# Kernel tuning notes

Hardware: AMD Instinct MI355X
Metric: run time of the kernel (lower is better)

Reference implementation:

```python
import jax, jax.numpy as jnp
import numpy as np

T, D_IN, D_OUT, E = 8192, 1024, 1024, 8
LN_EPS = 1e-5


def setup_inputs() -> dict:
    key = jax.random.key(0)
    k1, k2, k3 = jax.random.split(key, 3)
    x = jax.random.normal(k1, (T, D_IN), dtype=jnp.float32)
    # tokens are pre-sorted by expert; equal load => capacity = T // E per expert
    expert_frequency = jnp.full((E,), T // E, dtype=jnp.int64)
    # per-expert Linear(input_dim, output_dim) params
    W = jax.random.normal(k2, (E, D_IN, D_OUT), dtype=jnp.float32) / np.sqrt(D_IN)
    b = jax.random.normal(k3, (E, D_OUT), dtype=jnp.float32) * 0.02
    # per-expert LayerNorm(output_dim) affine params
    ln_gamma = jnp.ones((E, D_OUT), dtype=jnp.float32)
    ln_beta = jnp.zeros((E, D_OUT), dtype=jnp.float32)
    return {
        "expert_ordered_input": x,
        "expert_frequency": expert_frequency,
        "W": W,
        "b": b,
        "ln_gamma": ln_gamma,
        "ln_beta": ln_beta,
    }


def reference(expert_ordered_input, expert_frequency, W, b, ln_gamma, ln_beta):
    # Grouped-GEMM form of: split tokens by expert_frequency, apply per-expert
    # LayerBlock (Linear -> relu -> LayerNorm), then concat along token dim.
    # Frequencies are equal (capacity = T // E), so the ragged split is a reshape.
    x = expert_ordered_input
    n_tok, d_in = x.shape
    n_exp = W.shape[0]
    cap = n_tok // n_exp  # static capacity per expert
    xe = x.reshape(n_exp, cap, d_in)                       # [E, cap, d_in]
    h = jnp.einsum("ecd,edf->ecf", xe, W) + b[:, None, :]  # [E, cap, d_out]
    h = jax.nn.relu(h)
    mu = jnp.mean(h, axis=-1, keepdims=True)
    var = jnp.var(h, axis=-1, keepdims=True)
    hn = (h - mu) * jax.lax.rsqrt(var + LN_EPS)
    out = hn * ln_gamma[:, None, :] + ln_beta[:, None, :]
    return out.reshape(n_tok, -1)                          # concat over experts
```

## Files before the change

kernel.cpp:

```cpp
#include <hip/hip_runtime.h>
#include <hip/hip_bf16.h>
#include <stdint.h>

#define T_TOK 8192
#define DIN   1024
#define DOUT  1024
#define NEXP  8
#define CAP   1024
#define LN_EPS 1e-5f

#define BM 128
#define BN 128
#define BK 32
#define LDSS 48

typedef __attribute__((ext_vector_type(8))) short short8;
typedef __attribute__((ext_vector_type(4))) float f32x4;

__device__ __forceinline__ unsigned short f2bf(float f) {
    union { float f; unsigned int u; } v; v.f = f;
    unsigned int u = v.u;
    unsigned int r = u + 0x7FFFu + ((u >> 16) & 1u);
    return (unsigned short)(r >> 16);
}

__device__ __forceinline__ void gld16(void* l, const void* g) {
    __builtin_amdgcn_global_load_lds(
        (const __attribute__((address_space(1))) unsigned int*)(uintptr_t)g,
        (__attribute__((address_space(3))) unsigned int*)(uintptr_t)l,
        16, 0, 0);
}

__global__ __launch_bounds__(256) void xb_kernel(const float* __restrict__ X,
                                                 unsigned short* __restrict__ Xb) {
    int i = blockIdx.x * 256 + threadIdx.x;
    float4 v = ((const float4*)X)[i];
    ushort4 o;
    o.x = f2bf(v.x); o.y = f2bf(v.y); o.z = f2bf(v.z); o.w = f2bf(v.w);
    ((ushort4*)Xb)[i] = o;
}

__global__ __launch_bounds__(256) void wt_kernel(const float* __restrict__ W,
                                                 unsigned short* __restrict__ Wt) {
    __shared__ float tile[32][33];
    int e  = blockIdx.z;
    int k0 = blockIdx.y * 32;
    int n0 = blockIdx.x * 32;
    const float* Wp = W + (size_t)e * DIN * DOUT;
    unsigned short* Wtp = Wt + (size_t)e * DIN * DOUT;
    int tid = threadIdx.x;
    {
        int k  = tid >> 3;
        int c4 = tid & 7;
        float4 v = *(const float4*)(Wp + (size_t)(k0 + k) * DOUT + n0 + c4 * 4);
        tile[k][c4 * 4 + 0] = v.x; tile[k][c4 * 4 + 1] = v.y;
        tile[k][c4 * 4 + 2] = v.z; tile[k][c4 * 4 + 3] = v.w;
    }
    __syncthreads();
    {
        int n  = tid >> 3;
        int kc = tid & 7;
        ushort4 o;
        o.x = f2bf(tile[kc * 4 + 0][n]);
        o.y = f2bf(tile[kc * 4 + 1][n]);
        o.z = f2bf(tile[kc * 4 + 2][n]);
        o.w = f2bf(tile[kc * 4 + 3][n]);
        *(ushort4*)(Wtp + (size_t)(n0 + n) * DIN + k0 + kc * 4) = o;
    }
}

__global__ __launch_bounds__(256) void gemm2_kernel(
    const unsigned short* __restrict__ Xb,
    const unsigned short* __restrict__ Wt,
    const float* __restrict__ Bias,
    float* __restrict__ H)
{
    __shared__ unsigned short As[BM * BK];
    __shared__ unsigned short Bs[BN * BK];

    int blk = blockIdx.x;
    int e   = blk & 7;
    int m0  = (blk >> 6) * BM;
    int n0  = ((blk >> 3) & 7) * BN;

    int tid  = threadIdx.x;
    int wave = tid >> 6;
    int lane = tid & 63;
    int wm   = (wave >> 1) * 64;
    int wn   = (wave & 1) * 64;
    int lrow = lane & 15;
    int quad = lane >> 4;

    const unsigned short* Ag = Xb + (size_t)(e * CAP + m0) * DIN;
    const unsigned short* Bg = Wt + (size_t)e * DOUT * DIN + (size_t)n0 * DIN;

    int l0 = tid;
    int l1 = tid + 256;
    int ar0 = l0 >> 2, ac0 = (l0 & 3) * 8;
    int ar1 = l1 >> 2, ac1 = (l1 & 3) * 8;

    f32x4 acc[4][4];
#pragma unroll
    for (int i = 0; i < 4; i++)
#pragma unroll
        for (int j = 0; j < 4; j++)
            acc[i][j] = (f32x4)(0.0f);

    for (int k0 = 0; k0 < DIN; k0 += BK) {
        gld16(&As[l0 * 8], Ag + (size_t)ar0 * DIN + k0 + ac0);
        gld16(&As[l1 * 8], Ag + (size_t)ar1 * DIN + k0 + ac1);
        gld16(&Bs[l0 * 8], Bg + (size_t)ar0 * DIN + k0 + ac0);
        gld16(&Bs[l1 * 8], Bg + (size_t)ar1 * DIN + k0 + ac1);
        __syncthreads();

        short8 af[4], bf[4];
#pragma unroll
        for (int i = 0; i < 4; i++)
            af[i] = *(const short8*)&As[(wm + i * 16 + lrow) * BK + quad * 8];
#pragma unroll
        for (int j = 0; j < 4; j++)
            bf[j] = *(const short8*)&Bs[(wn + j * 16 + lrow) * BK + quad * 8];
#pragma unroll
        for (int i = 0; i < 4; i++)
#pragma unroll
            for (int j = 0; j < 4; j++)
                acc[i][j] = __builtin_amdgcn_mfma_f32_16x16x32_bf16(af[i], bf[j], acc[i][j], 0, 0, 0);
        __syncthreads();
    }

    float bias[4];
#pragma unroll
    for (int j = 0; j < 4; j++)
        bias[j] = Bias[e * DOUT + n0 + wn + j * 16 + lrow];

    int tok0 = e * CAP + m0 + wm;
#pragma unroll
    for (int i = 0; i < 4; i++) {
#pragma unroll
        for (int j = 0; j < 4; j++) {
            int col = n0 + wn + j * 16 + lrow;
#pragma unroll
            for (int r = 0; r < 4; r++) {
                int row = tok0 + i * 16 + quad * 4 + r;
                float v = acc[i][j][r] + bias[j];
                H[(size_t)row * DOUT + col] = fmaxf(v, 0.0f);
            }
        }
    }
}

__global__ __launch_bounds__(256, 2) void gemm_fb_kernel(
    const float* __restrict__ X,
    const unsigned short* __restrict__ Wt,
    const float* __restrict__ Bias,
    float* __restrict__ H)
{
    __shared__ unsigned short As[BM * LDSS];
    __shared__ unsigned short Bs[BN * LDSS];
    int blk = blockIdx.x;
    int e   = blk >> 6;
    int tt  = blk & 63;
    int m0  = (tt >> 3) * BM;
    int n0  = (tt & 7) * BN;
    int tid  = threadIdx.x;
    int wave = tid >> 6;
    int lane = tid & 63;
    int wm   = (wave >> 1) * 64;
    int wn   = (wave & 1) * 64;
    int lrow = lane & 15;
    int quad = lane >> 4;
    const float* Xe = X + (size_t)(e * CAP + m0) * DIN;
    const unsigned short* We = Wt + (size_t)e * DOUT * DIN + (size_t)n0 * DIN;
    f32x4 acc[4][4];
#pragma unroll
    for (int i = 0; i < 4; i++)
#pragma unroll
        for (int j = 0; j < 4; j++)
            acc[i][j] = (f32x4)(0.0f);
    for (int k0 = 0; k0 < DIN; k0 += BK) {
#pragma unroll
        for (int i = 0; i < 4; i++) {
            int idx = tid + i * 256;
            int row = idx >> 3;
            int c4  = idx & 7;
            const float4 xv = *(const float4*)(Xe + (size_t)row * DIN + k0 + c4 * 4);
            ushort4 bv;
            bv.x = f2bf(xv.x); bv.y = f2bf(xv.y); bv.z = f2bf(xv.z); bv.w = f2bf(xv.w);
            *(ushort4*)&As[row * LDSS + c4 * 4] = bv;
        }
#pragma unroll
        for (int i = 0; i < 2; i++) {
            int idx = tid + i * 256;
            int row = idx >> 2;
            int c   = idx & 3;
            uint4 wv = *(const uint4*)(We + (size_t)row * DIN + k0 + c * 8);
            *(uint4*)&Bs[row * LDSS + c * 8] = wv;
        }
        __syncthreads();
        short8 af[4], bf[4];
#pragma unroll
        for (int i = 0; i < 4; i++)
            af[i] = *(const short8*)&As[(wm + i * 16 + lrow) * LDSS + quad * 8];
#pragma unroll
        for (int j = 0; j < 4; j++)
            bf[j] = *(const short8*)&Bs[(wn + j * 16 + lrow) * LDSS + quad * 8];
#pragma unroll
        for (int i = 0; i < 4; i++)
#pragma unroll
            for (int j = 0; j < 4; j++)
                acc[i][j] = __builtin_amdgcn_mfma_f32_16x16x32_bf16(af[i], bf[j], acc[i][j], 0, 0, 0);
        __syncthreads();
    }
    float bias[4];
#pragma unroll
    for (int j = 0; j < 4; j++)
        bias[j] = Bias[e * DOUT + n0 + wn + j * 16 + lrow];
    int tok0 = e * CAP + m0 + wm;
#pragma unroll
    for (int i = 0; i < 4; i++)
#pragma unroll
        for (int j = 0; j < 4; j++) {
            int col = n0 + wn + j * 16 + lrow;
#pragma unroll
            for (int r = 0; r < 4; r++) {
                int row = tok0 + i * 16 + quad * 4 + r;
                float v = acc[i][j][r] + bias[j];
                H[(size_t)row * DOUT + col] = fmaxf(v, 0.0f);
            }
        }
}

__global__ __launch_bounds__(256) void ln_kernel(float* __restrict__ H,
                                                 const float* __restrict__ G,
                                                 const float* __restrict__ Bt) {
    int row = blockIdx.x;
    int e   = row >> 10;
    int tid  = threadIdx.x;
    int wave = tid >> 6;
    int lane = tid & 63;
    float* hp = H + (size_t)row * DOUT;

    float4 x = *(const float4*)(hp + tid * 4);
    float s  = x.x + x.y + x.z + x.w;
    float ss = fmaf(x.x, x.x, fmaf(x.y, x.y, fmaf(x.z, x.z, x.w * x.w)));
#pragma unroll
    for (int m = 32; m >= 1; m >>= 1) {
        s  += __shfl_xor(s, m);
        ss += __shfl_xor(ss, m);
    }
    __shared__ float red[8];
    if (lane == 0) { red[wave] = s; red[4 + wave] = ss; }
    __syncthreads();
    float ts  = red[0] + red[1] + red[2] + red[3];
    float tss = red[4] + red[5] + red[6] + red[7];
    float mean = ts * (1.0f / DOUT);
    float var  = fmaxf(tss * (1.0f / DOUT) - mean * mean, 0.0f);
    float rs = rsqrtf(var + LN_EPS);
    float4 g = *(const float4*)(G  + (size_t)e * DOUT + tid * 4);
    float4 b = *(const float4*)(Bt + (size_t)e * DOUT + tid * 4);
    float4 y;
    y.x = (x.x - mean) * rs * g.x + b.x;
    y.y = (x.y - mean) * rs * g.y + b.y;
    y.z = (x.z - mean) * rs * g.z + b.z;
    y.w = (x.w - mean) * rs * g.w + b.w;
    *(float4*)(hp + tid * 4) = y;
}

extern "C" void kernel_launch(void* const* d_in, const int* in_sizes, int n_in,
                              void* d_out, int out_size, void* d_ws, size_t ws_size,
                              hipStream_t stream) {
    const float* x  = (const float*)d_in[0];
    const float* W  = (const float*)d_in[2];
    const float* b  = (const float*)d_in[3];
    const float* g  = (const float*)d_in[4];
    const float* be = (const float*)d_in[5];
    float* out = (float*)d_out;

    unsigned short* Wt = (unsigned short*)d_ws;
    const size_t WT_BYTES = (size_t)NEXP * DIN * DOUT * 2;
    const size_t XB_BYTES = (size_t)T_TOK * DIN * 2;

    dim3 tb(256);
    wt_kernel<<<dim3(32, 32, 8), tb, 0, stream>>>(W, Wt);

    if (ws_size >= WT_BYTES + XB_BYTES) {
        unsigned short* Xb = (unsigned short*)((char*)d_ws + WT_BYTES);
        xb_kernel<<<dim3(8192), tb, 0, stream>>>(x, Xb);
        gemm2_kernel<<<dim3(512), tb, 0, stream>>>(Xb, Wt, b, out);
    } else {
        gemm_fb_kernel<<<dim3(512), tb, 0, stream>>>(x, Wt, b, out);
    }
    ln_kernel<<<dim3(8192), tb, 0, stream>>>(out, g, be);
}
```

Baseline: 153.0 us.

## Fuse LayerNorm into GEMM epilogue via atomic row stats and strip barrier

Merges the bf16 conversion of X and W plus zeroing of the stats buffers into one prep launch. The GEMM epilogue now applies bias and ReLU, accumulates per-row sum and sum-of-squares with atomics, and waits on a per-strip counter until all 8 N-tiles of that row strip have contributed. It then writes the normalized output directly, which removes the separate LayerNorm pass and the write and re-read of H. The inter-block spin-wait assumes all 8 blocks of a strip are co-resident (512 blocks at 2 per CU), so the code risks deadlock and adds atomic contention.

```diff
diff --git a/kernel.cpp b/kernel.cpp
--- a/kernel.cpp
+++ b/kernel.cpp
@@ -31,57 +31,70 @@
         16, 0, 0);
 }
 
-__global__ __launch_bounds__(256) void xb_kernel(const float* __restrict__ X,
-                                                 unsigned short* __restrict__ Xb) {
-    int i = blockIdx.x * 256 + threadIdx.x;
-    float4 v = ((const float4*)X)[i];
-    ushort4 o;
-    o.x = f2bf(v.x); o.y = f2bf(v.y); o.z = f2bf(v.z); o.w = f2bf(v.w);
-    ((ushort4*)Xb)[i] = o;
-}
-
-__global__ __launch_bounds__(256) void wt_kernel(const float* __restrict__ W,
-                                                 unsigned short* __restrict__ Wt) {
+__global__ __launch_bounds__(256) void prep_kernel(
+    const float* __restrict__ X, const float* __restrict__ W,
+    unsigned short* __restrict__ Xb, unsigned short* __restrict__ Wt,
+    float4* __restrict__ stats4, int* __restrict__ ctr) {
     __shared__ float tile[32][33];
-    int e  = blockIdx.z;
-    int k0 = blockIdx.y * 32;
-    int n0 = blockIdx.x * 32;
-    const float* Wp = W + (size_t)e * DIN * DOUT;
-    unsigned short* Wtp = Wt + (size_t)e * DIN * DOUT;
+    int blk = blockIdx.x;
     int tid = threadIdx.x;
-    {
-        int k  = tid >> 3;
-        int c4 = tid & 7;
-        float4 v = *(const float4*)(Wp + (size_t)(k0 + k) * DOUT + n0 + c4 * 4);
-        tile[k][c4 * 4 + 0] = v.x; tile[k][c4 * 4 + 1] = v.y;
-        tile[k][c4 * 4 + 2] = v.z; tile[k][c4 * 4 + 3] = v.w;
-    }
-    __syncthreads();
-    {
-        int n  = tid >> 3;
-        int kc = tid & 7;
+    if (blk < 8192) {
+        int i = blk * 256 + tid;
+        float4 v = ((const float4*)X)[i];
         ushort4 o;
-        o.x = f2bf(tile[kc * 4 + 0][n]);
-        o.y = f2bf(tile[kc * 4 + 1][n]);
-        o.z = f2bf(tile[kc * 4 + 2][n]);
-        o.w = f2bf(tile[kc * 4 + 3][n]);
-        *(ushort4*)(Wtp + (size_t)(n0 + n) * DIN + k0 + kc * 4) = o;
-    }
-}
-
-__global__ __launch_bounds__(256) void gemm2_kernel(
+        o.x = f2bf(v.x); o.y = f2bf(v.y); o.z = f2bf(v.z); o.w = f2bf(v.w);
+        ((ushort4*)Xb)[i] = o;
+    } else if (blk < 16384) {
+        int t  = blk - 8192;
+        int e  = t >> 10;
+        int k0 = ((t >> 5) & 31) * 32;
+        int n0 = (t & 31) * 32;
+        const float* Wp = W + (size_t)e * DIN * DOUT;
+        unsigned short* Wtp = Wt + (size_t)e * DIN * DOUT;
+        {
+            int k  = tid >> 3;
+            int c4 = tid & 7;
+            float4 v = *(const float4*)(Wp + (size_t)(k0 + k) * DOUT + n0 + c4 * 4);
+            tile[k][c4 * 4 + 0] = v.x; tile[k][c4 * 4 + 1] = v.y;
+            tile[k][c4 * 4 + 2] = v.z; tile[k][c4 * 4 + 3] = v.w;
+        }
+        __syncthreads();
+        {
+            int n  = tid >> 3;
+            int kc = tid & 7;
+            ushort4 o;
+            o.x = f2bf(tile[kc * 4 + 0][n]);
+            o.y = f2bf(tile[kc * 4 + 1][n]);
+            o.z = f2bf(tile[kc * 4 + 2][n]);
+            o.w = f2bf(tile[kc * 4 + 3][n]);
+            *(ushort4*)(Wtp + (size_t)(n0 + n) * DIN + k0 + kc * 4) = o;
+        }
+    } else {
+        int z = blk - 16384;
+        stats4[z * 256 + tid] = make_float4(0.f, 0.f, 0.f, 0.f);
+        if (z == 0 && tid < 64) ctr[tid] = 0;
+    }
+}
+
+__global__ __launch_bounds__(256, 2) void gemm3_kernel(
     const unsigned short* __restrict__ Xb,
     const unsigned short* __restrict__ Wt,
     const float* __restrict__ Bias,
-    float* __restrict__ H)
+    const float* __restrict__ G,
+    const float* __restrict__ Bt,
+    float* __restrict__ stats,
+    int* __restrict__ ctr,
+    float* __restrict__ Out)
 {
     __shared__ unsigned short As[BM * BK];
     __shared__ unsigned short Bs[BN * BK];
 
     int blk = blockIdx.x;
     int e   = blk & 7;
-    int m0  = (blk >> 6) * BM;
+    int mi  = blk >> 6;
+    int m0  = mi * BM;
     int n0  = ((blk >> 3) & 7) * BN;
+    int strip = e * 8 + mi;
 
     int tid  = threadIdx.x;
     int wave = tid >> 6;
@@ -128,32 +141,74 @@
         __syncthreads();
     }
 
-    float bias[4];
-#pragma unroll
-    for (int j = 0; j < 4; j++)
-        bias[j] = Bias[e * DOUT + n0 + wn + j * 16 + lrow];
+    float bias[4], gg[4], bb[4];
+#pragma unroll
+    for (int j = 0; j < 4; j++) {
+        int col = e * DOUT + n0 + wn + j * 16 + lrow;
+        bias[j] = Bias[col];
+        gg[j]   = G[col];
+        bb[j]   = Bt[col];
+    }
 
     int tok0 = e * CAP + m0 + wm;
+
 #pragma unroll
     for (int i = 0; i < 4; i++) {
 #pragma unroll
-        for (int j = 0; j < 4; j++) {
-            int col = n0 + wn + j * 16 + lrow;
-#pragma unroll
-            for (int r = 0; r < 4; r++) {
-                int row = tok0 + i * 16 + quad * 4 + r;
-                float v = acc[i][j][r] + bias[j];
-                H[(size_t)row * DOUT + col] = fmaxf(v, 0.0f);
+        for (int r = 0; r < 4; r++) {
+            float s = 0.f, ss = 0.f;
+#pragma unroll
+            for (int j = 0; j < 4; j++) {
+                float v = fmaxf(acc[i][j][r] + bias[j], 0.f);
+                acc[i][j][r] = v;
+                s += v;
+                ss = fmaf(v, v, ss);
+            }
+#pragma unroll
+            for (int m = 1; m <= 8; m <<= 1) {
+                s  += __shfl_xor(s, m);
+                ss += __shfl_xor(ss, m);
+            }
+            if (lrow == 0) {
+                int grow = tok0 + i * 16 + quad * 4 + r;
+                unsafeAtomicAdd(&stats[2 * grow],     s);
+                unsafeAtomicAdd(&stats[2 * grow + 1], ss);
+            }
+        }
+    }
+
+    __syncthreads();
+    if (tid == 0) {
+        __threadfence();
+        atomicAdd(&ctr[strip], 1);
+        while (atomicAdd(&ctr[strip], 0) < 8)
+            __builtin_amdgcn_s_sleep(8);
+    }
+    __syncthreads();
+    __threadfence();
+
+#pragma unroll
+    for (int i = 0; i < 4; i++) {
+#pragma unroll
+        for (int r = 0; r < 4; r++) {
+            int grow = tok0 + i * 16 + quad * 4 + r;
+            float su = stats[2 * grow];
+            float sq = stats[2 * grow + 1];
+            float mu  = su * (1.0f / DOUT);
+            float var = fmaxf(sq * (1.0f / DOUT) - mu * mu, 0.f);
+            float rs  = rsqrtf(var + LN_EPS);
+#pragma unroll
+            for (int j = 0; j < 4; j++) {
+                int gcol = n0 + wn + j * 16 + lrow;
+                Out[(size_t)grow * DOUT + gcol] = (acc[i][j][r] - mu) * rs * gg[j] + bb[j];
             }
         }
     }
 }
 
 __global__ __launch_bounds__(256, 2) void gemm_fb_kernel(
-    const float* __restrict__ X,
-    const unsigned short* __restrict__ Wt,
-    const float* __restrict__ Bias,
-    float* __restrict__ H)
+    const float* __restrict__ X, const unsigned short* __restrict__ Wt,
+    const float* __restrict__ Bias, float* __restrict__ H)
 {
     __shared__ unsigned short As[BM * LDSS];
     __shared__ unsigned short Bs[BN * LDSS];
@@ -239,7 +294,6 @@
     int wave = tid >> 6;
     int lane = tid & 63;
     float* hp = H + (size_t)row * DOUT;
-
     float4 x = *(const float4*)(hp + tid * 4);
     float s  = x.x + x.y + x.z + x.w;
     float ss = fmaf(x.x, x.x, fmaf(x.y, x.y, fmaf(x.z, x.z, x.w * x.w)));
@@ -266,6 +320,36 @@
     *(float4*)(hp + tid * 4) = y;
 }
 
+__global__ __launch_bounds__(256) void wt_only_kernel(const float* __restrict__ W,
+                                                      unsigned short* __restrict__ Wt) {
+    __shared__ float tile[32][33];
+    int t  = blockIdx.x;
+    int e  = t >> 10;
+    int k0 = ((t >> 5) & 31) * 32;
+    int n0 = (t & 31) * 32;
+    int tid = threadIdx.x;
+    const float* Wp = W + (size_t)e * DIN * DOUT;
+    unsigned short* Wtp = Wt + (size_t)e * DIN * DOUT;
+    {
+        int k  = tid >> 3;
+        int c4 = tid & 7;
+        float4 v = *(const float4*)(Wp + (size_t)(k0 + k) * DOUT + n0 + c4 * 4);
+        tile[k][c4 * 4 + 0] = v.x; tile[k][c4 * 4 + 1] = v.y;
+        tile[k][c4 * 4 + 2] = v.z; tile[k][c4 * 4 + 3] = v.w;
+    }
+    __syncthreads();
+    {
+        int n  = tid >> 3;
+        int kc = tid & 7;
+        ushort4 o;
+        o.x = f2bf(tile[kc * 4 + 0][n]);
+        o.y = f2bf(tile[kc * 4 + 1][n]);
+        o.z = f2bf(tile[kc * 4 + 2][n]);
+        o.w = f2bf(tile[kc * 4 + 3][n]);
+        *(ushort4*)(Wtp + (size_t)(n0 + n) * DIN + k0 + kc * 4) = o;
+    }
+}
+
 extern "C" void kernel_launch(void* const* d_in, const int* in_sizes, int n_in,
                               void* d_out, int out_size, void* d_ws, size_t ws_size,
                               hipStream_t stream) {
@@ -276,19 +360,23 @@
     const float* be = (const float*)d_in[5];
     float* out = (float*)d_out;
 
-    unsigned short* Wt = (unsigned short*)d_ws;
     const size_t WT_BYTES = (size_t)NEXP * DIN * DOUT * 2;
     const size_t XB_BYTES = (size_t)T_TOK * DIN * 2;
-
+    const size_t ST_BYTES = (size_t)T_TOK * 2 * 4;
+    const size_t NEEDED   = WT_BYTES + XB_BYTES + ST_BYTES + 256;
+
+    unsigned short* Wt = (unsigned short*)d_ws;
     dim3 tb(256);
-    wt_kernel<<<dim3(32, 32, 8), tb, 0, stream>>>(W, Wt);
-
-    if (ws_size >= WT_BYTES + XB_BYTES) {
+
+    if (ws_size >= NEEDED) {
         unsigned short* Xb = (unsigned short*)((char*)d_ws + WT_BYTES);
-        xb_kernel<<<dim3(8192), tb, 0, stream>>>(x, Xb);
-        gemm2_kernel<<<dim3(512), tb, 0, stream>>>(Xb, Wt, b, out);
+        float* stats = (float*)((char*)d_ws + WT_BYTES + XB_BYTES);
+        int* ctr = (int*)((char*)d_ws + WT_BYTES + XB_BYTES + ST_BYTES);
+        prep_kernel<<<dim3(16400), tb, 0, stream>>>(x, W, Xb, Wt, (float4*)stats, ctr);
+        gemm3_kernel<<<dim3(512), tb, 0, stream>>>(Xb, Wt, b, g, be, stats, ctr, out);
     } else {
+        wt_only_kernel<<<dim3(8192), tb, 0, stream>>>(W, Wt);
         gemm_fb_kernel<<<dim3(512), tb, 0, stream>>>(x, Wt, b, out);
-    }
-    ln_kernel<<<dim3(8192), tb, 0, stream>>>(out, g, be);
-}
+        ln_kernel<<<dim3(8192), tb, 0, stream>>>(out, g, be);
+    }
+}
```

Measured after the change: 188.3 us. +23.1%, slower.
